# Optimization experiments

Hardware: AMD Instinct MI355X
Metric: run time of the kernel (lower is better)

Reference implementation:

```python
import jax, jax.numpy as jnp
import numpy as np

K_TOP = 2  # top-k experts per token (MoE k)


def setup_inputs() -> dict:
    key = jax.random.key(0)
    ks = jax.random.split(key, 4)
    B, D, H, E = 4096, 1024, 2048, 8
    x = jax.random.normal(ks[0], (B, D), dtype=jnp.float32)
    w_gate = jax.random.normal(ks[1], (D, E), dtype=jnp.float32) * 0.02
    W1 = jax.random.normal(ks[2], (E, D, H), dtype=jnp.float32) * (1.0 / np.sqrt(D))
    b1 = jnp.zeros((E, H), dtype=jnp.float32)
    W2 = jax.random.normal(ks[3], (E, H, D), dtype=jnp.float32) * (1.0 / np.sqrt(H))
    b2 = jnp.zeros((E, D), dtype=jnp.float32)
    return {"x": x, "w_gate": w_gate, "W1": W1, "b1": b1, "W2": W2, "b2": b2}


def _top_k_gates(logits, k):
    # noisy_top_k_gating, eval path (noisy_gating=False / train=False):
    # softmax over the top-k logits, scattered back to [B, E]; other gates are 0.
    B, E = logits.shape
    top_logits, top_idx = jax.lax.top_k(logits, k)       # [B, k]
    top_gates = jax.nn.softmax(top_logits, axis=-1)      # [B, k]
    rows = jnp.arange(B)[:, None]
    gates = jnp.zeros((B, E), dtype=logits.dtype).at[rows, top_idx].set(top_gates)
    return gates


def reference(x, w_gate, W1, b1, W2, b2):
    # Gating
    logits = x @ w_gate                                  # [B, E]
    gates = _top_k_gates(logits, K_TOP)                  # [B, E], sparse (top-k nonzero)
    # Experts: MLP(fc1 -> relu -> fc2) per expert. Dense-all-experts form is
    # mathematically identical to dispatch/combine since zero gates contribute 0.
    h = jax.nn.relu(jnp.einsum('bd,edh->beh', x, W1) + b1[None])   # [B, E, H]
    y = jnp.einsum('beh,ehd->bed', h, W2) + b2[None]               # [B, E, D]
    out = jnp.einsum('be,bed->bd', gates, y)                       # gated scatter-combine
    return out
```

## Files before the change

### kernel.cpp

```cpp
#include <hip/hip_runtime.h>

#define B_TOK 4096
#define DDIM  1024
#define HDIM  2048
#define NEXP  8
#define MAXTOK 4096
#define BM 128
#define BN 128
#define BK 64

#define OFF_W1T  0ull
#define OFF_W2T  33554432ull
#define OFF_XB   67108864ull
#define OFF_H    75497472ull
#define OFF_Y    109051904ull
#define OFF_TOK  125829120ull
#define OFF_GATE 125960192ull
#define OFF_PAIR 126091264ull
#define OFF_CNT  126124032ull
#define OFF_OFFS 126124096ull
#define OFF_EIDX (OFF_Y)
#define OFF_GCO  (OFF_Y + 16384ull)

typedef __attribute__((ext_vector_type(4))) float f32x4;
typedef __attribute__((ext_vector_type(8))) short bf16x8;

static __device__ __forceinline__ unsigned short f2bf(float f) {
    unsigned u = __builtin_bit_cast(unsigned, f);
    unsigned r = (u + 0x7FFFu + ((u >> 16) & 1u)) >> 16;
    return (unsigned short)r;
}
static __device__ __forceinline__ float bf2f(unsigned short s) {
    unsigned u = ((unsigned)s) << 16;
    return __builtin_bit_cast(float, u);
}

#define AS1(p) ((const __attribute__((address_space(1))) void*)(p))
#define AS3(p) ((__attribute__((address_space(3))) void*)(p))

__global__ void __launch_bounds__(256) gating_logits_kernel(
    const float* __restrict__ x, const float* __restrict__ wg,
    int* __restrict__ eidx, float* __restrict__ gco, short* __restrict__ Xb) {
    int wave = threadIdx.x >> 6;
    int lane = threadIdx.x & 63;
    int b = blockIdx.x * 4 + wave;
    float acc[NEXP];
#pragma unroll
    for (int e = 0; e < NEXP; e++) acc[e] = 0.f;
    const float* xr = x + (size_t)b * DDIM;
    short* xbr = Xb + (size_t)b * DDIM;
#pragma unroll
    for (int i = 0; i < DDIM / 64; i++) {
        int d = i * 64 + lane;
        float xv = xr[d];
        xbr[d] = (short)f2bf(xv);
        const float4* wrow = (const float4*)(wg + (size_t)d * NEXP);
        float4 w0 = wrow[0], w1 = wrow[1];
        acc[0] += xv * w0.x; acc[1] += xv * w0.y; acc[2] += xv * w0.z; acc[3] += xv * w0.w;
        acc[4] += xv * w1.x; acc[5] += xv * w1.y; acc[6] += xv * w1.z; acc[7] += xv * w1.w;
    }
#pragma unroll
    for (int off = 32; off >= 1; off >>= 1)
#pragma unroll
        for (int e = 0; e < NEXP; e++) acc[e] += __shfl_xor(acc[e], off);
    if (lane == 0) {
        int i1 = 0; float m1 = acc[0];
        for (int e = 1; e < NEXP; e++) if (acc[e] > m1) { m1 = acc[e]; i1 = e; }
        int i2 = (i1 == 0) ? 1 : 0; float m2 = -1e30f;
        for (int e = 0; e < NEXP; e++) { if (e == i1) continue; if (acc[e] > m2) { m2 = acc[e]; i2 = e; } }
        float g1 = 1.f / (1.f + expf(m2 - m1));
        eidx[b] = i1 | (i2 << 16);
        gco[b] = g1;
    }
}

__global__ void __launch_bounds__(256) build_kernel(
    const int* __restrict__ eidx, const float* __restrict__ gco,
    int* __restrict__ counts, int* __restrict__ tok,
    float* __restrict__ gate, int* __restrict__ pair) {
    __shared__ int lhist[NEXP];
    __shared__ int gbase[NEXP];
    int t = threadIdx.x;
    if (t < NEXP) lhist[t] = 0;
    __syncthreads();
    int b = blockIdx.x * 256 + t;
    int ep = eidx[b];
    int e1 = ep & 0xffff, e2 = ep >> 16;
    float g1 = gco[b], g2 = 1.f - g1;
    int l1 = atomicAdd(&lhist[e1], 1);
    int l2 = atomicAdd(&lhist[e2], 1);
    __syncthreads();
    if (t < NEXP) gbase[t] = atomicAdd(&counts[t], lhist[t]);
    __syncthreads();
    int s1 = gbase[e1] + l1, s2 = gbase[e2] + l2;
    tok[e1 * MAXTOK + s1] = b; gate[e1 * MAXTOK + s1] = g1; pair[b * 2 + 0] = e1 * MAXTOK + s1;
    tok[e2 * MAXTOK + s2] = b; gate[e2 * MAXTOK + s2] = g2; pair[b * 2 + 1] = e2 * MAXTOK + s2;
}

__global__ void scan_kernel(const int* __restrict__ counts, int* __restrict__ offs) {
    if (threadIdx.x == 0) {
        int s = 0;
        for (int e = 0; e < NEXP; e++) { offs[e] = s; s += counts[e]; }
    }
}

__global__ void __launch_bounds__(256) tcvt_kernel(const float* __restrict__ src, short* __restrict__ dst,
                                                   int R, int C) {
    __shared__ float tile[64][65];
    int e = blockIdx.z;
    size_t base = (size_t)e * R * C;
    int r0 = blockIdx.y * 64, c0 = blockIdx.x * 64;
    int t = threadIdx.x;
    int rr = t >> 4, c4 = (t & 15) * 4;
    const float* s = src + base + (size_t)r0 * C + c0;
#pragma unroll
    for (int i = 0; i < 4; i++) {
        float4 v = *(const float4*)(s + (size_t)(rr + i * 16) * C + c4);
        tile[rr + i * 16][c4 + 0] = v.x; tile[rr + i * 16][c4 + 1] = v.y;
        tile[rr + i * 16][c4 + 2] = v.z; tile[rr + i * 16][c4 + 3] = v.w;
    }
    __syncthreads();
    short* d = dst + base + (size_t)c0 * R + r0;
    int hr0 = t >> 4, dc = (t & 15) * 4;
#pragma unroll
    for (int i = 0; i < 4; i++) {
        int hr = hr0 + i * 16;
        short4 o;
        o.x = (short)f2bf(tile[dc + 0][hr]); o.y = (short)f2bf(tile[dc + 1][hr]);
        o.z = (short)f2bf(tile[dc + 2][hr]); o.w = (short)f2bf(tile[dc + 3][hr]);
        *(short4*)(d + (size_t)hr * R + dc) = o;
    }
}

__global__ void __launch_bounds__(256, 3) fc1_kernel(
    const short* __restrict__ Xb, const short* __restrict__ W1T, const float* __restrict__ b1,
    short* __restrict__ h, const int* __restrict__ tok,
    const int* __restrict__ counts, const int* __restrict__ offs) {
    int bid = blockIdx.x;
    int e = bid & 7;
    int r2 = bid >> 3;
    int m0 = (r2 & 31) * BM;
    int n0 = (r2 >> 5) * BN;
    int cnt = counts[e];
    if (m0 >= cnt) return;
    int baseh = offs[e];

    __shared__ short As[BM * BK];
    __shared__ short Bs[BN * BK];

    int t = threadIdx.x;
    int wave = t >> 6, lane = t & 63;

    const short* asrc[4]; const short* bsrc[4];
    int dsto[4];
#pragma unroll
    for (int i = 0; i < 4; i++) {
        int G = i * 256 + t;
        int r = G >> 3, q = G & 7;
        int cks = ((q ^ (r & 7)) << 3);
        int trow = m0 + r;
        int tid2 = (trow < cnt) ? tok[e * MAXTOK + trow] : 0;
        asrc[i] = Xb + (size_t)tid2 * DDIM + cks;
        bsrc[i] = W1T + ((size_t)e * HDIM + n0 + r) * DDIM + cks;
        dsto[i] = G * 8;
    }

    int wr = (wave >> 1) * 64, wc = (wave & 1) * 64;
    f32x4 acc[4][4];
    f32x4 zero = {0.f, 0.f, 0.f, 0.f};
#pragma unroll
    for (int m = 0; m < 4; m++)
#pragma unroll
        for (int n = 0; n < 4; n++) acc[m][n] = zero;

    int l15 = lane & 15, l7 = lane & 7, lhi = lane >> 4;
    int aoff[4][2], boff[4][2];
#pragma unroll
    for (int ks = 0; ks < 2; ks++) {
        int q = (lhi + ks * 4) ^ l7;
#pragma unroll
        for (int m = 0; m < 4; m++) {
            aoff[m][ks] = (wr + m * 16 + l15) * BK + (q << 3);
            boff[m][ks] = (wc + m * 16 + l15) * BK + (q << 3);
        }
    }

    const int NT = DDIM / BK;
    for (int kt = 0; kt < NT; ++kt) {
        int k0 = kt * BK;
#pragma unroll
        for (int i = 0; i < 4; i++) {
            __builtin_amdgcn_global_load_lds(AS1(asrc[i] + k0), AS3(&As[dsto[i]]), 16, 0, 0);
            __builtin_amdgcn_global_load_lds(AS1(bsrc[i] + k0), AS3(&Bs[dsto[i]]), 16, 0, 0);
        }
        __syncthreads();
#pragma unroll
        for (int ks = 0; ks < 2; ks++) {
            bf16x8 af[4], bg[4];
#pragma unroll
            for (int m = 0; m < 4; m++) {
                af[m] = *(const bf16x8*)(&As[aoff[m][ks]]);
                bg[m] = *(const bf16x8*)(&Bs[boff[m][ks]]);
            }
            __builtin_amdgcn_s_setprio(1);
#pragma unroll
            for (int m = 0; m < 4; m++)
#pragma unroll
                for (int n = 0; n < 4; n++)
                    acc[m][n] = __builtin_amdgcn_mfma_f32_16x16x32_bf16(bg[n], af[m], acc[m][n], 0, 0, 0);
            __builtin_amdgcn_s_setprio(0);
        }
        __syncthreads();
    }

#pragma unroll
    for (int m = 0; m < 4; m++) {
        int row = m0 + wr + m * 16 + l15;
        if (row < cnt) {
            size_t rb = (size_t)(baseh + row) * HDIM;
#pragma unroll
            for (int n = 0; n < 4; n++) {
                int colb = n0 + wc + n * 16 + (lhi << 2);
                float4 bias = *(const float4*)(b1 + e * HDIM + colb);
                float v0 = acc[m][n][0] + bias.x; v0 = v0 > 0.f ? v0 : 0.f;
                float v1 = acc[m][n][1] + bias.y; v1 = v1 > 0.f ? v1 : 0.f;
                float v2 = acc[m][n][2] + bias.z; v2 = v2 > 0.f ? v2 : 0.f;
                float v3 = acc[m][n][3] + bias.w; v3 = v3 > 0.f ? v3 : 0.f;
                short4 o;
                o.x = (short)f2bf(v0); o.y = (short)f2bf(v1);
                o.z = (short)f2bf(v2); o.w = (short)f2bf(v3);
                *(short4*)(h + rb + colb) = o;
            }
        }
    }
}

__global__ void __launch_bounds__(256, 3) fc2_kernel(
    const short* __restrict__ h, const short* __restrict__ W2T, const float* __restrict__ b2,
    short* __restrict__ ybuf, const int* __restrict__ counts, const int* __restrict__ offs) {
    int bid = blockIdx.x;
    int e = bid & 7;
    int r2 = bid >> 3;
    int m0 = (r2 & 31) * BM;
    int n0 = (r2 >> 5) * BN;
    int cnt = counts[e];
    if (m0 >= cnt) return;
    int baseh = offs[e];

    __shared__ short As[BM * BK];
    __shared__ short Bs[BN * BK];

    int t = threadIdx.x;
    int wave = t >> 6, lane = t & 63;

    const short* asrc[4]; const short* bsrc[4];
    int dsto[4];
#pragma unroll
    for (int i = 0; i < 4; i++) {
        int G = i * 256 + t;
        int r = G >> 3, q = G & 7;
        int cks = ((q ^ (r & 7)) << 3);
        asrc[i] = h + (size_t)(baseh + m0 + r) * HDIM + cks;
        bsrc[i] = W2T + ((size_t)e * DDIM + n0 + r) * HDIM + cks;
        dsto[i] = G * 8;
    }

    int wr = (wave >> 1) * 64, wc = (wave & 1) * 64;
    f32x4 acc[4][4];
    f32x4 zero = {0.f, 0.f, 0.f, 0.f};
#pragma unroll
    for (int m = 0; m < 4; m++)
#pragma unroll
        for (int n = 0; n < 4; n++) acc[m][n] = zero;

    int l15 = lane & 15, l7 = lane & 7, lhi = lane >> 4;
    int aoff[4][2], boff[4][2];
#pragma unroll
    for (int ks = 0; ks < 2; ks++) {
        int q = (lhi + ks * 4) ^ l7;
#pragma unroll
        for (int m = 0; m < 4; m++) {
            aoff[m][ks] = (wr + m * 16 + l15) * BK + (q << 3);
            boff[m][ks] = (wc + m * 16 + l15) * BK + (q << 3);
        }
    }

    const int NT = HDIM / BK;
    for (int kt = 0; kt < NT; ++kt) {
        int k0 = kt * BK;
#pragma unroll
        for (int i = 0; i < 4; i++) {
            __builtin_amdgcn_global_load_lds(AS1(asrc[i] + k0), AS3(&As[dsto[i]]), 16, 0, 0);
            __builtin_amdgcn_global_load_lds(AS1(bsrc[i] + k0), AS3(&Bs[dsto[i]]), 16, 0, 0);
        }
        __syncthreads();
#pragma unroll
        for (int ks = 0; ks < 2; ks++) {
            bf16x8 af[4], bg[4];
#pragma unroll
            for (int m = 0; m < 4; m++) {
                af[m] = *(const bf16x8*)(&As[aoff[m][ks]]);
                bg[m] = *(const bf16x8*)(&Bs[boff[m][ks]]);
            }
            __builtin_amdgcn_s_setprio(1);
#pragma unroll
            for (int m = 0; m < 4; m++)
#pragma unroll
                for (int n = 0; n < 4; n++)
                    acc[m][n] = __builtin_amdgcn_mfma_f32_16x16x32_bf16(bg[n], af[m], acc[m][n], 0, 0, 0);
            __builtin_amdgcn_s_setprio(0);
        }
        __syncthreads();
    }

#pragma unroll
    for (int m = 0; m < 4; m++) {
        int row = m0 + wr + m * 16 + l15;
        if (row < cnt) {
            size_t rb = (size_t)(baseh + row) * DDIM;
#pragma unroll
            for (int n = 0; n < 4; n++) {
                int colb = n0 + wc + n * 16 + (lhi << 2);
                float4 bias = *(const float4*)(b2 + e * DDIM + colb);
                short4 o;
                o.x = (short)f2bf(acc[m][n][0] + bias.x);
                o.y = (short)f2bf(acc[m][n][1] + bias.y);
                o.z = (short)f2bf(acc[m][n][2] + bias.z);
                o.w = (short)f2bf(acc[m][n][3] + bias.w);
                *(short4*)(ybuf + rb + colb) = o;
            }
        }
    }
}

__global__ void __launch_bounds__(256) combine_kernel(
    const short* __restrict__ ybuf, const float* __restrict__ gate,
    const int* __restrict__ pair, const int* __restrict__ offs, float* __restrict__ out) {
    int b = blockIdx.x;
    int p0 = pair[b * 2], p1 = pair[b * 2 + 1];
    float g0 = gate[p0], g1 = gate[p1];
    int r0 = offs[p0 >> 12] + (p0 & 4095);
    int r1 = offs[p1 >> 12] + (p1 & 4095);
    const short4* y0 = (const short4*)(ybuf + (size_t)r0 * DDIM);
    const short4* y1 = (const short4*)(ybuf + (size_t)r1 * DDIM);
    float4* o = (float4*)(out + (size_t)b * DDIM);
    int t = threadIdx.x;
    short4 a = y0[t], c = y1[t];
    float4 v;
    v.x = g0 * bf2f((unsigned short)a.x) + g1 * bf2f((unsigned short)c.x);
    v.y = g0 * bf2f((unsigned short)a.y) + g1 * bf2f((unsigned short)c.y);
    v.z = g0 * bf2f((unsigned short)a.z) + g1 * bf2f((unsigned short)c.z);
    v.w = g0 * bf2f((unsigned short)a.w) + g1 * bf2f((unsigned short)c.w);
    o[t] = v;
}

extern "C" void kernel_launch(void* const* d_in, const int* in_sizes, int n_in,
                              void* d_out, int out_size, void* d_ws, size_t ws_size,
                              hipStream_t stream) {
    const float* x  = (const float*)d_in[0];
    const float* wg = (const float*)d_in[1];
    const float* W1 = (const float*)d_in[2];
    const float* b1 = (const float*)d_in[3];
    const float* W2 = (const float*)d_in[4];
    const float* b2 = (const float*)d_in[5];
    float* out = (float*)d_out;
    char* ws = (char*)d_ws;

    short* W1T = (short*)(ws + OFF_W1T);
    short* W2T = (short*)(ws + OFF_W2T);
    short* Xb  = (short*)(ws + OFF_XB);
    short* h   = (short*)(ws + OFF_H);
    short* ybuf = (short*)(ws + OFF_Y);
    int* tok   = (int*)(ws + OFF_TOK);
    float* gate = (float*)(ws + OFF_GATE);
    int* pair  = (int*)(ws + OFF_PAIR);
    int* counts = (int*)(ws + OFF_CNT);
    int* offs  = (int*)(ws + OFF_OFFS);
    int* eidx  = (int*)(ws + OFF_EIDX);
    float* gco = (float*)(ws + OFF_GCO);

    hipMemsetAsync(counts, 0, 64, stream);
    gating_logits_kernel<<<B_TOK / 4, 256, 0, stream>>>(x, wg, eidx, gco, Xb);
    build_kernel<<<B_TOK / 256, 256, 0, stream>>>(eidx, gco, counts, tok, gate, pair);
    scan_kernel<<<1, 64, 0, stream>>>(counts, offs);
    tcvt_kernel<<<dim3(HDIM / 64, DDIM / 64, NEXP), 256, 0, stream>>>(W1, W1T, DDIM, HDIM);
    tcvt_kernel<<<dim3(DDIM / 64, HDIM / 64, NEXP), 256, 0, stream>>>(W2, W2T, HDIM, DDIM);
    fc1_kernel<<<NEXP * 32 * (HDIM / BN), 256, 0, stream>>>(Xb, W1T, b1, h, tok, counts, offs);
    fc2_kernel<<<NEXP * 32 * (DDIM / BN), 256, 0, stream>>>(h, W2T, b2, ybuf, counts, offs);
    combine_kernel<<<B_TOK, 256, 0, stream>>>(ybuf, gate, pair, offs, out);
}
```

Before: 187.4 us.

## Double-buffer LDS tiles in fc1 and fc2 GEMM main loops

Both expert GEMM kernels now keep two LDS buffers for the A and B tiles. Each iteration issues the async global-to-LDS loads for the next K tile before running the MFMAs on the current one, so memory latency can overlap with compute. The barrier at the end of each iteration both waits for the prefetch and protects buffer reuse, which removes one barrier per iteration. LDS per block doubles to 64 KB, and the occupancy hint in launch_bounds drops from 3 to 2 blocks per CU, so less latency is hidden by running blocks concurrently.

```diff
diff --git a/kernel.cpp b/kernel.cpp
--- a/kernel.cpp
+++ b/kernel.cpp
@@ -132,7 +132,7 @@
     }
 }
 
-__global__ void __launch_bounds__(256, 3) fc1_kernel(
+__global__ void __launch_bounds__(256, 2) fc1_kernel(
     const short* __restrict__ Xb, const short* __restrict__ W1T, const float* __restrict__ b1,
     short* __restrict__ h, const int* __restrict__ tok,
     const int* __restrict__ counts, const int* __restrict__ offs) {
@@ -145,8 +145,8 @@
     if (m0 >= cnt) return;
     int baseh = offs[e];
 
-    __shared__ short As[BM * BK];
-    __shared__ short Bs[BN * BK];
+    __shared__ short As[2][BM * BK];
+    __shared__ short Bs[2][BN * BK];
 
     int t = threadIdx.x;
     int wave = t >> 6, lane = t & 63;
@@ -185,22 +185,27 @@
         }
     }
 
+#define STAGE1(buf, k0) do { \
+    _Pragma("unroll") \
+    for (int i = 0; i < 4; i++) { \
+        __builtin_amdgcn_global_load_lds(AS1(asrc[i] + (k0)), AS3(&As[buf][dsto[i]]), 16, 0, 0); \
+        __builtin_amdgcn_global_load_lds(AS1(bsrc[i] + (k0)), AS3(&Bs[buf][dsto[i]]), 16, 0, 0); \
+    } \
+} while (0)
+
+    STAGE1(0, 0);
+    __syncthreads();
+    int cur = 0;
     const int NT = DDIM / BK;
     for (int kt = 0; kt < NT; ++kt) {
-        int k0 = kt * BK;
-#pragma unroll
-        for (int i = 0; i < 4; i++) {
-            __builtin_amdgcn_global_load_lds(AS1(asrc[i] + k0), AS3(&As[dsto[i]]), 16, 0, 0);
-            __builtin_amdgcn_global_load_lds(AS1(bsrc[i] + k0), AS3(&Bs[dsto[i]]), 16, 0, 0);
-        }
-        __syncthreads();
+        if (kt < NT - 1) STAGE1(cur ^ 1, (kt + 1) * BK);
 #pragma unroll
         for (int ks = 0; ks < 2; ks++) {
             bf16x8 af[4], bg[4];
 #pragma unroll
             for (int m = 0; m < 4; m++) {
-                af[m] = *(const bf16x8*)(&As[aoff[m][ks]]);
-                bg[m] = *(const bf16x8*)(&Bs[boff[m][ks]]);
+                af[m] = *(const bf16x8*)(&As[cur][aoff[m][ks]]);
+                bg[m] = *(const bf16x8*)(&Bs[cur][boff[m][ks]]);
             }
             __builtin_amdgcn_s_setprio(1);
 #pragma unroll
@@ -211,7 +216,9 @@
             __builtin_amdgcn_s_setprio(0);
         }
         __syncthreads();
-    }
+        cur ^= 1;
+    }
+#undef STAGE1
 
 #pragma unroll
     for (int m = 0; m < 4; m++) {
@@ -235,7 +242,7 @@
     }
 }
 
-__global__ void __launch_bounds__(256, 3) fc2_kernel(
+__global__ void __launch_bounds__(256, 2) fc2_kernel(
     const short* __restrict__ h, const short* __restrict__ W2T, const float* __restrict__ b2,
     short* __restrict__ ybuf, const int* __restrict__ counts, const int* __restrict__ offs) {
     int bid = blockIdx.x;
@@ -247,8 +254,8 @@
     if (m0 >= cnt) return;
     int baseh = offs[e];
 
-    __shared__ short As[BM * BK];
-    __shared__ short Bs[BN * BK];
+    __shared__ short As[2][BM * BK];
+    __shared__ short Bs[2][BN * BK];
 
     int t = threadIdx.x;
     int wave = t >> 6, lane = t & 63;
@@ -285,22 +292,27 @@
         }
     }
 
+#define STAGE2(buf, k0) do { \
+    _Pragma("unroll") \
+    for (int i = 0; i < 4; i++) { \
+        __builtin_amdgcn_global_load_lds(AS1(asrc[i] + (k0)), AS3(&As[buf][dsto[i]]), 16, 0, 0); \
+        __builtin_amdgcn_global_load_lds(AS1(bsrc[i] + (k0)), AS3(&Bs[buf][dsto[i]]), 16, 0, 0); \
+    } \
+} while (0)
+
+    STAGE2(0, 0);
+    __syncthreads();
+    int cur = 0;
     const int NT = HDIM / BK;
     for (int kt = 0; kt < NT; ++kt) {
-        int k0 = kt * BK;
-#pragma unroll
-        for (int i = 0; i < 4; i++) {
-            __builtin_amdgcn_global_load_lds(AS1(asrc[i] + k0), AS3(&As[dsto[i]]), 16, 0, 0);
-            __builtin_amdgcn_global_load_lds(AS1(bsrc[i] + k0), AS3(&Bs[dsto[i]]), 16, 0, 0);
-        }
-        __syncthreads();
+        if (kt < NT - 1) STAGE2(cur ^ 1, (kt + 1) * BK);
 #pragma unroll
         for (int ks = 0; ks < 2; ks++) {
             bf16x8 af[4], bg[4];
 #pragma unroll
             for (int m = 0; m < 4; m++) {
-                af[m] = *(const bf16x8*)(&As[aoff[m][ks]]);
-                bg[m] = *(const bf16x8*)(&Bs[boff[m][ks]]);
+                af[m] = *(const bf16x8*)(&As[cur][aoff[m][ks]]);
+                bg[m] = *(const bf16x8*)(&Bs[cur][boff[m][ks]]);
             }
             __builtin_amdgcn_s_setprio(1);
 #pragma unroll
@@ -311,7 +323,9 @@
             __builtin_amdgcn_s_setprio(0);
         }
         __syncthreads();
-    }
+        cur ^= 1;
+    }
+#undef STAGE2
 
 #pragma unroll
     for (int m = 0; m < 4; m++) {
```

Result: slower. 199.2 us (+6.3%).

## Enlarge expert GEMM tiles to 256x256 with 512-thread blocks

Applied to the files above, without the earlier changes.

Changes the fc1 and fc2 grouped GEMM kernels from 128x128 tiles with 4 waves to 256x256 tiles with 8 waves, each wave computing a 128x64 sub-tile. The aim is to raise arithmetic intensity and cut redundant global and LDS loads of the weight and activation tiles. In exchange, accumulator registers double per thread, LDS per block grows to 64KB, and more work is wasted on partially filled M tiles for experts with uneven token counts. Fewer blocks per expert may also lower occupancy and load balance.

```diff
diff --git a/kernel.cpp b/kernel.cpp
--- a/kernel.cpp
+++ b/kernel.cpp
@@ -5,8 +5,6 @@
 #define HDIM  2048
 #define NEXP  8
 #define MAXTOK 4096
-#define BM 128
-#define BN 128
 #define BK 64
 
 #define OFF_W1T  0ull
@@ -132,21 +130,21 @@
     }
 }
 
-__global__ void __launch_bounds__(256, 3) fc1_kernel(
+__global__ void __launch_bounds__(512, 2) fc1_kernel(
     const short* __restrict__ Xb, const short* __restrict__ W1T, const float* __restrict__ b1,
     short* __restrict__ h, const int* __restrict__ tok,
     const int* __restrict__ counts, const int* __restrict__ offs) {
     int bid = blockIdx.x;
     int e = bid & 7;
     int r2 = bid >> 3;
-    int m0 = (r2 & 31) * BM;
-    int n0 = (r2 >> 5) * BN;
+    int m0 = (r2 & 15) * 256;
+    int n0 = (r2 >> 4) * 256;
     int cnt = counts[e];
     if (m0 >= cnt) return;
     int baseh = offs[e];
 
-    __shared__ short As[BM * BK];
-    __shared__ short Bs[BN * BK];
+    __shared__ short As[256 * BK];
+    __shared__ short Bs[256 * BK];
 
     int t = threadIdx.x;
     int wave = t >> 6, lane = t & 63;
@@ -155,7 +153,7 @@
     int dsto[4];
 #pragma unroll
     for (int i = 0; i < 4; i++) {
-        int G = i * 256 + t;
+        int G = i * 512 + t;
         int r = G >> 3, q = G & 7;
         int cks = ((q ^ (r & 7)) << 3);
         int trow = m0 + r;
@@ -165,24 +163,23 @@
         dsto[i] = G * 8;
     }
 
-    int wr = (wave >> 1) * 64, wc = (wave & 1) * 64;
-    f32x4 acc[4][4];
+    int wr2 = (wave >> 2) * 128, wc2 = (wave & 3) * 64;
+    f32x4 acc[8][4];
     f32x4 zero = {0.f, 0.f, 0.f, 0.f};
 #pragma unroll
-    for (int m = 0; m < 4; m++)
+    for (int m = 0; m < 8; m++)
 #pragma unroll
         for (int n = 0; n < 4; n++) acc[m][n] = zero;
 
     int l15 = lane & 15, l7 = lane & 7, lhi = lane >> 4;
-    int aoff[4][2], boff[4][2];
+    int aoff[8][2], boff[4][2];
 #pragma unroll
     for (int ks = 0; ks < 2; ks++) {
         int q = (lhi + ks * 4) ^ l7;
 #pragma unroll
-        for (int m = 0; m < 4; m++) {
-            aoff[m][ks] = (wr + m * 16 + l15) * BK + (q << 3);
-            boff[m][ks] = (wc + m * 16 + l15) * BK + (q << 3);
-        }
+        for (int m = 0; m < 8; m++) aoff[m][ks] = (wr2 + m * 16 + l15) * BK + (q << 3);
+#pragma unroll
+        for (int n = 0; n < 4; n++) boff[n][ks] = (wc2 + n * 16 + l15) * BK + (q << 3);
     }
 
     const int NT = DDIM / BK;
@@ -196,15 +193,14 @@
         __syncthreads();
 #pragma unroll
         for (int ks = 0; ks < 2; ks++) {
-            bf16x8 af[4], bg[4];
-#pragma unroll
-            for (int m = 0; m < 4; m++) {
-                af[m] = *(const bf16x8*)(&As[aoff[m][ks]]);
-                bg[m] = *(const bf16x8*)(&Bs[boff[m][ks]]);
-            }
+            bf16x8 af[8], bg[4];
+#pragma unroll
+            for (int m = 0; m < 8; m++) af[m] = *(const bf16x8*)(&As[aoff[m][ks]]);
+#pragma unroll
+            for (int n = 0; n < 4; n++) bg[n] = *(const bf16x8*)(&Bs[boff[n][ks]]);
             __builtin_amdgcn_s_setprio(1);
 #pragma unroll
-            for (int m = 0; m < 4; m++)
+            for (int m = 0; m < 8; m++)
 #pragma unroll
                 for (int n = 0; n < 4; n++)
                     acc[m][n] = __builtin_amdgcn_mfma_f32_16x16x32_bf16(bg[n], af[m], acc[m][n], 0, 0, 0);
@@ -214,13 +210,13 @@
     }
 
 #pragma unroll
-    for (int m = 0; m < 4; m++) {
-        int row = m0 + wr + m * 16 + l15;
+    for (int m = 0; m < 8; m++) {
+        int row = m0 + wr2 + m * 16 + l15;
         if (row < cnt) {
             size_t rb = (size_t)(baseh + row) * HDIM;
 #pragma unroll
             for (int n = 0; n < 4; n++) {
-                int colb = n0 + wc + n * 16 + (lhi << 2);
+                int colb = n0 + wc2 + n * 16 + (lhi << 2);
                 float4 bias = *(const float4*)(b1 + e * HDIM + colb);
                 float v0 = acc[m][n][0] + bias.x; v0 = v0 > 0.f ? v0 : 0.f;
                 float v1 = acc[m][n][1] + bias.y; v1 = v1 > 0.f ? v1 : 0.f;
@@ -235,20 +231,20 @@
     }
 }
 
-__global__ void __launch_bounds__(256, 3) fc2_kernel(
+__global__ void __launch_bounds__(512, 2) fc2_kernel(
     const short* __restrict__ h, const short* __restrict__ W2T, const float* __restrict__ b2,
     short* __restrict__ ybuf, const int* __restrict__ counts, const int* __restrict__ offs) {
     int bid = blockIdx.x;
     int e = bid & 7;
     int r2 = bid >> 3;
-    int m0 = (r2 & 31) * BM;
-    int n0 = (r2 >> 5) * BN;
+    int m0 = (r2 & 15) * 256;
+    int n0 = (r2 >> 4) * 256;
     int cnt = counts[e];
     if (m0 >= cnt) return;
     int baseh = offs[e];
 
-    __shared__ short As[BM * BK];
-    __shared__ short Bs[BN * BK];
+    __shared__ short As[256 * BK];
+    __shared__ short Bs[256 * BK];
 
     int t = threadIdx.x;
     int wave = t >> 6, lane = t & 63;
@@ -257,7 +253,7 @@
     int dsto[4];
 #pragma unroll
     for (int i = 0; i < 4; i++) {
-        int G = i * 256 + t;
+        int G = i * 512 + t;
         int r = G >> 3, q = G & 7;
         int cks = ((q ^ (r & 7)) << 3);
         asrc[i] = h + (size_t)(baseh + m0 + r) * HDIM + cks;
@@ -265,24 +261,23 @@
         dsto[i] = G * 8;
     }
 
-    int wr = (wave >> 1) * 64, wc = (wave & 1) * 64;
-    f32x4 acc[4][4];
+    int wr2 = (wave >> 2) * 128, wc2 = (wave & 3) * 64;
+    f32x4 acc[8][4];
     f32x4 zero = {0.f, 0.f, 0.f, 0.f};
 #pragma unroll
-    for (int m = 0; m < 4; m++)
+    for (int m = 0; m < 8; m++)
 #pragma unroll
         for (int n = 0; n < 4; n++) acc[m][n] = zero;
 
     int l15 = lane & 15, l7 = lane & 7, lhi = lane >> 4;
-    int aoff[4][2], boff[4][2];
+    int aoff[8][2], boff[4][2];
 #pragma unroll
     for (int ks = 0; ks < 2; ks++) {
         int q = (lhi + ks * 4) ^ l7;
 #pragma unroll
-        for (int m = 0; m < 4; m++) {
-            aoff[m][ks] = (wr + m * 16 + l15) * BK + (q << 3);
-            boff[m][ks] = (wc + m * 16 + l15) * BK + (q << 3);
-        }
+        for (int m = 0; m < 8; m++) aoff[m][ks] = (wr2 + m * 16 + l15) * BK + (q << 3);
+#pragma unroll
+        for (int n = 0; n < 4; n++) boff[n][ks] = (wc2 + n * 16 + l15) * BK + (q << 3);
     }
 
     const int NT = HDIM / BK;
@@ -296,15 +291,14 @@
         __syncthreads();
 #pragma unroll
         for (int ks = 0; ks < 2; ks++) {
-            bf16x8 af[4], bg[4];
-#pragma unroll
-            for (int m = 0; m < 4; m++) {
-                af[m] = *(const bf16x8*)(&As[aoff[m][ks]]);
-                bg[m] = *(const bf16x8*)(&Bs[boff[m][ks]]);
-            }
+            bf16x8 af[8], bg[4];
+#pragma unroll
+            for (int m = 0; m < 8; m++) af[m] = *(const bf16x8*)(&As[aoff[m][ks]]);
+#pragma unroll
+            for (int n = 0; n < 4; n++) bg[n] = *(const bf16x8*)(&Bs[boff[n][ks]]);
             __builtin_amdgcn_s_setprio(1);
 #pragma unroll
-            for (int m = 0; m < 4; m++)
+            for (int m = 0; m < 8; m++)
 #pragma unroll
                 for (int n = 0; n < 4; n++)
                     acc[m][n] = __builtin_amdgcn_mfma_f32_16x16x32_bf16(bg[n], af[m], acc[m][n], 0, 0, 0);
@@ -314,13 +308,13 @@
     }
 
 #pragma unroll
-    for (int m = 0; m < 4; m++) {
-        int row = m0 + wr + m * 16 + l15;
+    for (int m = 0; m < 8; m++) {
+        int row = m0 + wr2 + m * 16 + l15;
         if (row < cnt) {
             size_t rb = (size_t)(baseh + row) * DDIM;
 #pragma unroll
             for (int n = 0; n < 4; n++) {
-                int colb = n0 + wc + n * 16 + (lhi << 2);
+                int colb = n0 + wc2 + n * 16 + (lhi << 2);
                 float4 bias = *(const float4*)(b2 + e * DDIM + colb);
                 short4 o;
                 o.x = (short)f2bf(acc[m][n][0] + bias.x);
@@ -385,7 +379,7 @@
     scan_kernel<<<1, 64, 0, stream>>>(counts, offs);
     tcvt_kernel<<<dim3(HDIM / 64, DDIM / 64, NEXP), 256, 0, stream>>>(W1, W1T, DDIM, HDIM);
     tcvt_kernel<<<dim3(DDIM / 64, HDIM / 64, NEXP), 256, 0, stream>>>(W2, W2T, HDIM, DDIM);
-    fc1_kernel<<<NEXP * 32 * (HDIM / BN), 256, 0, stream>>>(Xb, W1T, b1, h, tok, counts, offs);
-    fc2_kernel<<<NEXP * 32 * (DDIM / BN), 256, 0, stream>>>(h, W2T, b2, ybuf, counts, offs);
+    fc1_kernel<<<NEXP * (MAXTOK / 256) * (HDIM / 256), 512, 0, stream>>>(Xb, W1T, b1, h, tok, counts, offs);
+    fc2_kernel<<<NEXP * (MAXTOK / 256) * (DDIM / 256), 512, 0, stream>>>(h, W2T, b2, ybuf, counts, offs);
     combine_kernel<<<B_TOK, 256, 0, stream>>>(ybuf, gate, pair, offs, out);
 }
```

Result: slower. 226.3 us (+20.7%).
